# Kernel optimization log

Measured on AMD Instinct MI355X. Metric: run time of the kernel, lower is better.

The kernel has to match this reference:

```python
import jax, jax.numpy as jnp
import numpy as np

B, L, P, A = 32, 512, 128, 128   # batch, prot seq len, prot dim, atom dim
N = 1024                          # total atoms (32 per molecule)
H1, H2 = 512, 256                 # hidden_list


def setup_inputs() -> dict:
    key = jax.random.key(0)
    ks = jax.random.split(key, 12)
    atom_embed = jax.random.normal(ks[0], (N, A), dtype=jnp.float32)
    protSeq_embed = jax.random.normal(ks[1], (B, L, P), dtype=jnp.float32)
    # sorted segment ids, every segment non-empty (32 atoms per molecule)
    atom_splits = jnp.repeat(jnp.arange(B, dtype=jnp.int64), N // B)
    s = 0.05
    att1_W = jax.random.normal(ks[2], (P + A, 128), dtype=jnp.float32) * s
    att1_b = jnp.zeros((128,), dtype=jnp.float32)
    att2_W = jax.random.normal(ks[3], (128, 1), dtype=jnp.float32) * s
    att2_b = jnp.zeros((1,), dtype=jnp.float32)
    d1_W = jax.random.normal(ks[4], (A + P, H1), dtype=jnp.float32) * s
    d1_b = jnp.zeros((H1,), dtype=jnp.float32)
    d2_W = jax.random.normal(ks[5], (H1, H2), dtype=jnp.float32) * s
    d2_b = jnp.zeros((H2,), dtype=jnp.float32)
    out_W = jax.random.normal(ks[6], (H2, 1), dtype=jnp.float32) * s
    out_b = jnp.zeros((1,), dtype=jnp.float32)
    return {"atom_embed": atom_embed, "protSeq_embed": protSeq_embed,
            "atom_splits": atom_splits,
            "att1_W": att1_W, "att1_b": att1_b, "att2_W": att2_W, "att2_b": att2_b,
            "d1_W": d1_W, "d1_b": d1_b, "d2_W": d2_W, "d2_b": d2_b,
            "out_W": out_W, "out_b": out_b}


def reference(atom_embed, protSeq_embed, atom_splits,
              att1_W, att1_b, att2_W, att2_b,
              d1_W, d1_b, d2_W, d2_b, out_W, out_b):
    num_seg = protSeq_embed.shape[0]
    # gather protein rows per atom: [N, L, P]
    prot_g = protSeq_embed[atom_splits]
    # concat with broadcast atom embed: [N, L, P+A]
    atom_x = jnp.broadcast_to(atom_embed[:, None, :], prot_g.shape[:2] + atom_embed.shape[-1:])
    concat = jnp.concatenate([prot_g, atom_x], axis=-1)
    # attention MLP -> scores W: [N, L]
    hid = jnp.tanh(concat @ att1_W + att1_b)
    W = 5.0 * jnp.tanh(hid @ att2_W + att2_b)[..., 0]
    # atom-side weights: exp(max over seq), normalized per segment
    Wc = jnp.exp(jnp.max(W, axis=-1, keepdims=True))                     # [N, 1]
    Sc = jax.ops.segment_sum(Wc, atom_splits, num_segments=num_seg)[atom_splits]
    aa = Wc / Sc                                                          # [N, 1]
    atom_pool = jax.ops.segment_sum(aa * atom_embed, atom_splits, num_segments=num_seg)  # [B, A]
    # protein-side: segment-max scores, softmax over seq, weighted sum
    Wp = jax.ops.segment_max(W, atom_splits, num_segments=num_seg)       # [B, L]
    ap = jax.nn.softmax(Wp, axis=-1)
    prot_pool = jnp.einsum('bl,bld->bd', ap, protSeq_embed)              # [B, P]
    z = jnp.concatenate([atom_pool, prot_pool], axis=-1)
    z = jax.nn.relu(z @ d1_W + d1_b)
    z = jax.nn.relu(z @ d2_W + d2_b)
    return z @ out_W + out_b                                             # [B, 1]
```

## Files before the change

### kernel.cpp

```cpp
#include <hip/hip_runtime.h>
#include <math.h>

#define BSEG 32
#define LSEQ 512

__device__ __forceinline__ float fast_tanh(float x) {
    x = fminf(fmaxf(x, -20.0f), 20.0f);
    float e = __expf(2.0f * x);
    return __fdividef(e - 1.0f, e + 1.0f);
}
__device__ __forceinline__ float trm(float c, float p, float e) {
    return c * __builtin_amdgcn_rcpf(fmaf(p, e, 1.0f));
}
__device__ __forceinline__ float clexp2(float v) {
    return __expf(2.0f * fminf(fmaxf(v, -20.0f), 20.0f));
}

__device__ __forceinline__ void gemm32_exp(
    const float* __restrict__ Xrow0, const float* __restrict__ Wm,
    const float* __restrict__ bias, float* __restrict__ xs,
    float* __restrict__ ws, float* __restrict__ dst, int tid)
{
    #pragma unroll
    for (int t = 0; t < 4; ++t) {
        int flat = (tid + 256 * t) * 4;
        int r = flat >> 7, k4 = flat & 127;
        *(float4*)&xs[r * 132 + k4] = *(const float4*)&Xrow0[r * 128 + k4];
    }
    const int tx = tid & 31, ty = tid >> 5;
    float acc[4][4];
    #pragma unroll
    for (int i = 0; i < 4; ++i)
        #pragma unroll
        for (int j = 0; j < 4; ++j) acc[i][j] = 0.0f;
    #pragma unroll
    for (int q = 0; q < 4; ++q) {
        #pragma unroll
        for (int t = 0; t < 4; ++t) {
            int flat = (tid + 256 * t) * 4;
            int kk = flat >> 7, c4 = flat & 127;
            *(float4*)&ws[kk * 132 + c4] =
                *(const float4*)&Wm[(q * 32 + kk) * 128 + c4];
        }
        __syncthreads();
        #pragma unroll 4
        for (int kk = 0; kk < 32; ++kk) {
            float4 b4 = *(const float4*)&ws[kk * 132 + 4 * tx];
            int k = q * 32 + kk;
            float a0 = xs[(4 * ty + 0) * 132 + k];
            float a1 = xs[(4 * ty + 1) * 132 + k];
            float a2 = xs[(4 * ty + 2) * 132 + k];
            float a3 = xs[(4 * ty + 3) * 132 + k];
            acc[0][0] += a0 * b4.x; acc[0][1] += a0 * b4.y;
            acc[0][2] += a0 * b4.z; acc[0][3] += a0 * b4.w;
            acc[1][0] += a1 * b4.x; acc[1][1] += a1 * b4.y;
            acc[1][2] += a1 * b4.z; acc[1][3] += a1 * b4.w;
            acc[2][0] += a2 * b4.x; acc[2][1] += a2 * b4.y;
            acc[2][2] += a2 * b4.z; acc[2][3] += a2 * b4.w;
            acc[3][0] += a3 * b4.x; acc[3][1] += a3 * b4.y;
            acc[3][2] += a3 * b4.z; acc[3][3] += a3 * b4.w;
        }
        __syncthreads();
    }
    float b4v[4] = {0.f, 0.f, 0.f, 0.f};
    if (bias) *(float4*)b4v = *(const float4*)&bias[4 * tx];
    #pragma unroll
    for (int i = 0; i < 4; ++i) {
        float4 o;
        o.x = clexp2(acc[i][0] + b4v[0]);
        o.y = clexp2(acc[i][1] + b4v[1]);
        o.z = clexp2(acc[i][2] + b4v[2]);
        o.w = clexp2(acc[i][3] + b4v[3]);
        *(float4*)&dst[(4 * ty + i) * 132 + 4 * tx] = o;
    }
}

__global__ __launch_bounds__(256, 2) void fused_kernel(
    const float* __restrict__ atom_embed, const float* __restrict__ protSeq,
    const float* __restrict__ att1_W, const float* __restrict__ att1_b,
    const float* __restrict__ att2_W, const float* __restrict__ att2_b,
    const float* __restrict__ out_b,
    float* __restrict__ pmax, float* __restrict__ zrp,
    float* __restrict__ dpp, float* __restrict__ out)
{
    __shared__ float smem[16896];
    float* eps = smem;
    float* ebs = smem + 4224;
    float* xs  = smem + 8448;
    float* ws  = smem + 12672;
    float* c_s  = smem + 8448;
    float* pmn  = smem + 8576;
    float* wps  = smem + 9664;
    float* es   = smem + 9696;
    float* part = smem + 9728;
    float* scal = smem + 9984;

    const int tid = threadIdx.x;
    const int chunk = blockIdx.x, b = blockIdx.y;
    const int lbase = chunk * 32;

    if (chunk == 0 && tid == 0) out[b] = out_b[0];

    gemm32_exp(protSeq + ((long)(b * 512 + lbase)) * 128, att1_W, att1_b,
               xs, ws, eps, tid);
    gemm32_exp(atom_embed + (long)b * 32 * 128, att1_W + 128 * 128, nullptr,
               xs, ws, ebs, tid);

    if (tid < 128) c_s[tid] = -2.0f * att2_W[tid];
    __syncthreads();
    if (tid < 64) {
        float s = c_s[tid] + c_s[tid + 64];
        #pragma unroll
        for (int m = 1; m < 64; m <<= 1) s += __shfl_xor(s, m);
        if (tid == 0) scal[0] = -0.5f * s + att2_b[0];
    }
    __syncthreads();

    const int ng = tid & 7, lg = tid >> 3;
    const float* qp  = &eps[lg * 132];
    const float* b0p = &ebs[ng * 132];
    const float* b1p = &ebs[(ng + 8) * 132];
    const float* b2p = &ebs[(ng + 16) * 132];
    const float* b3p = &ebs[(ng + 24) * 132];
    float a0 = 0.f, a1 = 0.f, a2 = 0.f, a3 = 0.f;
    #pragma unroll 4
    for (int jj = 0; jj < 128; jj += 4) {
        float4 c4 = *(const float4*)&c_s[jj];
        float4 q  = *(const float4*)(qp + jj);
        float4 b0 = *(const float4*)(b0p + jj);
        float4 b1 = *(const float4*)(b1p + jj);
        float4 b2 = *(const float4*)(b2p + jj);
        float4 b3 = *(const float4*)(b3p + jj);
        a0 += trm(c4.x, q.x, b0.x); a1 += trm(c4.x, q.x, b1.x);
        a2 += trm(c4.x, q.x, b2.x); a3 += trm(c4.x, q.x, b3.x);
        a0 += trm(c4.y, q.y, b0.y); a1 += trm(c4.y, q.y, b1.y);
        a2 += trm(c4.y, q.y, b2.y); a3 += trm(c4.y, q.y, b3.y);
        a0 += trm(c4.z, q.z, b0.z); a1 += trm(c4.z, q.z, b1.z);
        a2 += trm(c4.z, q.z, b2.z); a3 += trm(c4.z, q.z, b3.z);
        a0 += trm(c4.w, q.w, b0.w); a1 += trm(c4.w, q.w, b1.w);
        a2 += trm(c4.w, q.w, b2.w); a3 += trm(c4.w, q.w, b3.w);
    }
    const float bs = scal[0];
    float W0 = 5.0f * fast_tanh(a0 + bs);
    float W1 = 5.0f * fast_tanh(a1 + bs);
    float W2 = 5.0f * fast_tanh(a2 + bs);
    float W3 = 5.0f * fast_tanh(a3 + bs);

    float m = fmaxf(fmaxf(W0, W1), fmaxf(W2, W3));
    #pragma unroll
    for (int d = 1; d < 8; d <<= 1) m = fmaxf(m, __shfl_xor(m, d));
    if (ng == 0) wps[lg] = m;
    pmn[lg * 34 + ng]      = W0;
    pmn[lg * 34 + ng + 8]  = W1;
    pmn[lg * 34 + ng + 16] = W2;
    pmn[lg * 34 + ng + 24] = W3;
    __syncthreads();
    if (tid < 32) {
        float mm = pmn[tid];
        #pragma unroll
        for (int g = 1; g < 32; ++g) mm = fmaxf(mm, pmn[g * 34 + tid]);
        pmax[b * 512 + chunk * 32 + tid] = mm;
        es[tid] = __expf(wps[tid]);
    }
    __syncthreads();
    if (tid < 32) {
        float v = es[tid];
        #pragma unroll
        for (int d = 1; d < 32; d <<= 1) v += __shfl_xor(v, d);
        if (tid == 0) dpp[b * 16 + chunk] = v;
    }
    const int dd = tid & 127, hf = tid >> 7;
    float az = 0.0f;
    #pragma unroll 4
    for (int i = 0; i < 16; ++i)
        az += es[hf * 16 + i] *
              protSeq[((long)(b * 512 + lbase + hf * 16 + i)) * 128 + dd];
    part[tid] = az;
    __syncthreads();
    if (tid < 128) zrp[(b * 16 + chunk) * 128 + tid] = part[tid] + part[128 + tid];
}

__global__ __launch_bounds__(256) void mlp1_kernel(
    const float* __restrict__ pmax, const float* __restrict__ zrp,
    const float* __restrict__ dpp, const float* __restrict__ atom_embed,
    const float* __restrict__ d1_W, const float* __restrict__ d1_b,
    float* __restrict__ h1)
{
    __shared__ float zs[256];
    __shared__ float part[4 * 65];
    __shared__ float expw[32];
    __shared__ float sc[2];
    const int tid = threadIdx.x;
    const int cx = blockIdx.x, b = blockIdx.y;

    if (tid < 32) {
        float m = -1e30f;
        #pragma unroll
        for (int c = 0; c < 16; ++c) m = fmaxf(m, pmax[b * 512 + c * 32 + tid]);
        float e = __expf(m);
        expw[tid] = e;
        #pragma unroll
        for (int d = 1; d < 32; d <<= 1) e += __shfl_xor(e, d);
        if (tid == 0) sc[0] = 1.0f / e;
    }
    if (tid == 64) {
        float s = 0.0f;
        #pragma unroll
        for (int c = 0; c < 16; ++c) s += dpp[b * 16 + c];
        sc[1] = 1.0f / s;
    }
    __syncthreads();
    if (tid < 128) {
        float a = 0.0f;
        #pragma unroll 8
        for (int n = 0; n < 32; ++n)
            a += expw[n] * atom_embed[(b * 32 + n) * 128 + tid];
        zs[tid] = a * sc[0];
    } else {
        int d = tid - 128;
        float a = 0.0f;
        #pragma unroll
        for (int c = 0; c < 16; ++c) a += zrp[(b * 16 + c) * 128 + d];
        zs[tid] = a * sc[1];
    }
    __syncthreads();
    const int c0 = cx * 64, ci = tid & 63, kg = tid >> 6;
    float acc = 0.0f;
    #pragma unroll 8
    for (int k = kg * 64; k < kg * 64 + 64; ++k)
        acc += zs[k] * d1_W[k * 512 + c0 + ci];
    part[kg * 65 + ci] = acc;
    __syncthreads();
    if (tid < 64) {
        float s = part[tid] + part[65 + tid] + part[130 + tid] + part[195 + tid]
                + d1_b[c0 + tid];
        h1[b * 512 + c0 + tid] = fmaxf(s, 0.0f);
    }
}

__global__ __launch_bounds__(256) void mlp2_kernel(
    const float* __restrict__ h1, const float* __restrict__ d2_W,
    const float* __restrict__ d2_b, const float* __restrict__ out_W,
    float* __restrict__ out)
{
    __shared__ float hs[512];
    __shared__ float part[8 * 33];
    const int tid = threadIdx.x;
    const int c0 = blockIdx.x * 32, b = blockIdx.y;
    hs[tid] = h1[b * 512 + tid];
    hs[tid + 256] = h1[b * 512 + 256 + tid];
    __syncthreads();
    const int ci = tid & 31, kg = tid >> 5;
    float acc = 0.0f;
    #pragma unroll 8
    for (int k = kg * 64; k < kg * 64 + 64; ++k)
        acc += hs[k] * d2_W[k * 256 + c0 + ci];
    part[kg * 33 + ci] = acc;
    __syncthreads();
    if (tid < 32) {
        float s = d2_b[c0 + tid];
        #pragma unroll
        for (int g = 0; g < 8; ++g) s += part[g * 33 + tid];
        float contrib = fmaxf(s, 0.0f) * out_W[c0 + tid];
        #pragma unroll
        for (int d = 1; d < 32; d <<= 1) contrib += __shfl_xor(contrib, d);
        if (tid == 0) atomicAdd(&out[b], contrib);
    }
}

extern "C" void kernel_launch(void* const* d_in, const int* in_sizes, int n_in,
                              void* d_out, int out_size, void* d_ws, size_t ws_size,
                              hipStream_t stream) {
    const float* atom_embed = (const float*)d_in[0];
    const float* protSeq    = (const float*)d_in[1];
    const float* att1_W = (const float*)d_in[3];
    const float* att1_b = (const float*)d_in[4];
    const float* att2_W = (const float*)d_in[5];
    const float* att2_b = (const float*)d_in[6];
    const float* d1_W   = (const float*)d_in[7];
    const float* d1_b   = (const float*)d_in[8];
    const float* d2_W   = (const float*)d_in[9];
    const float* d2_b   = (const float*)d_in[10];
    const float* out_W  = (const float*)d_in[11];
    const float* out_b  = (const float*)d_in[12];
    float* out = (float*)d_out;

    float* ws = (float*)d_ws;
    float* pmax = ws;
    float* zrp  = pmax + 16384;
    float* dpp  = zrp + 65536;
    float* h1   = dpp + 512;

    fused_kernel<<<dim3(16, BSEG), 256, 0, stream>>>(
        atom_embed, protSeq, att1_W, att1_b, att2_W, att2_b, out_b,
        pmax, zrp, dpp, out);
    mlp1_kernel<<<dim3(8, BSEG), 256, 0, stream>>>(
        pmax, zrp, dpp, atom_embed, d1_W, d1_b, h1);
    mlp2_kernel<<<dim3(8, BSEG), 256, 0, stream>>>(
        h1, d2_W, d2_b, out_W, out);
}
```

Measured before the change: 123.9 us.

## Hoist atom-side attention GEMM into separate kernel and vectorize LDS A loads

The atom-embedding half of the first attention layer was recomputed by each of the 16 chunk blocks per molecule. It is now computed once per molecule in a new eb_kernel, written to workspace, and loaded by fused_kernel. Separately, the inner GEMM loop now reads A values from shared memory as float4 over groups of four k values, cutting the number of LDS instructions. The cost is an extra kernel launch and a global-memory round trip for the 128x1024 intermediate.

```diff
diff --git a/kernel.cpp b/kernel.cpp
--- a/kernel.cpp
+++ b/kernel.cpp
@@ -19,7 +19,7 @@
 __device__ __forceinline__ void gemm32_exp(
     const float* __restrict__ Xrow0, const float* __restrict__ Wm,
     const float* __restrict__ bias, float* __restrict__ xs,
-    float* __restrict__ ws, float* __restrict__ dst, int tid)
+    float* __restrict__ ws, float* __restrict__ dst, int dstride, int tid)
 {
     #pragma unroll
     for (int t = 0; t < 4; ++t) {
@@ -43,22 +43,22 @@
                 *(const float4*)&Wm[(q * 32 + kk) * 128 + c4];
         }
         __syncthreads();
-        #pragma unroll 4
-        for (int kk = 0; kk < 32; ++kk) {
-            float4 b4 = *(const float4*)&ws[kk * 132 + 4 * tx];
-            int k = q * 32 + kk;
-            float a0 = xs[(4 * ty + 0) * 132 + k];
-            float a1 = xs[(4 * ty + 1) * 132 + k];
-            float a2 = xs[(4 * ty + 2) * 132 + k];
-            float a3 = xs[(4 * ty + 3) * 132 + k];
-            acc[0][0] += a0 * b4.x; acc[0][1] += a0 * b4.y;
-            acc[0][2] += a0 * b4.z; acc[0][3] += a0 * b4.w;
-            acc[1][0] += a1 * b4.x; acc[1][1] += a1 * b4.y;
-            acc[1][2] += a1 * b4.z; acc[1][3] += a1 * b4.w;
-            acc[2][0] += a2 * b4.x; acc[2][1] += a2 * b4.y;
-            acc[2][2] += a2 * b4.z; acc[2][3] += a2 * b4.w;
-            acc[3][0] += a3 * b4.x; acc[3][1] += a3 * b4.y;
-            acc[3][2] += a3 * b4.z; acc[3][3] += a3 * b4.w;
+        #pragma unroll 2
+        for (int kg = 0; kg < 8; ++kg) {
+            float4 A[4];
+            #pragma unroll
+            for (int r = 0; r < 4; ++r)
+                A[r] = *(const float4*)&xs[(4 * ty + r) * 132 + q * 32 + kg * 4];
+            #pragma unroll
+            for (int j = 0; j < 4; ++j) {
+                float4 b4 = *(const float4*)&ws[(kg * 4 + j) * 132 + 4 * tx];
+                #pragma unroll
+                for (int r = 0; r < 4; ++r) {
+                    float av = ((const float*)&A[r])[j];
+                    acc[r][0] += av * b4.x; acc[r][1] += av * b4.y;
+                    acc[r][2] += av * b4.z; acc[r][3] += av * b4.w;
+                }
+            }
         }
         __syncthreads();
     }
@@ -71,12 +71,22 @@
         o.y = clexp2(acc[i][1] + b4v[1]);
         o.z = clexp2(acc[i][2] + b4v[2]);
         o.w = clexp2(acc[i][3] + b4v[3]);
-        *(float4*)&dst[(4 * ty + i) * 132 + 4 * tx] = o;
-    }
+        *(float4*)&dst[(4 * ty + i) * dstride + 4 * tx] = o;
+    }
+}
+
+__global__ __launch_bounds__(256) void eb_kernel(
+    const float* __restrict__ atom_embed, const float* __restrict__ Wa,
+    float* __restrict__ eb)
+{
+    __shared__ float smem[8448];
+    const int b = blockIdx.x;
+    gemm32_exp(atom_embed + (long)b * 32 * 128, Wa, nullptr,
+               smem, smem + 4224, eb + (long)b * 32 * 128, 128, threadIdx.x);
 }
 
 __global__ __launch_bounds__(256, 2) void fused_kernel(
-    const float* __restrict__ atom_embed, const float* __restrict__ protSeq,
+    const float* __restrict__ eb, const float* __restrict__ protSeq,
     const float* __restrict__ att1_W, const float* __restrict__ att1_b,
     const float* __restrict__ att2_W, const float* __restrict__ att2_b,
     const float* __restrict__ out_b,
@@ -101,10 +111,15 @@
 
     if (chunk == 0 && tid == 0) out[b] = out_b[0];
 
+    #pragma unroll
+    for (int t = 0; t < 4; ++t) {
+        int flat = (tid + 256 * t) * 4;
+        int n = flat >> 7, j = flat & 127;
+        *(float4*)&ebs[n * 132 + j] = *(const float4*)&eb[(b * 32 + n) * 128 + j];
+    }
+
     gemm32_exp(protSeq + ((long)(b * 512 + lbase)) * 128, att1_W, att1_b,
-               xs, ws, eps, tid);
-    gemm32_exp(atom_embed + (long)b * 32 * 128, att1_W + 128 * 128, nullptr,
-               xs, ws, ebs, tid);
+               xs, ws, eps, 132, tid);
 
     if (tid < 128) c_s[tid] = -2.0f * att2_W[tid];
     __syncthreads();
@@ -286,13 +301,15 @@
     float* out = (float*)d_out;
 
     float* ws = (float*)d_ws;
-    float* pmax = ws;
+    float* eb   = ws;
+    float* pmax = eb + 131072;
     float* zrp  = pmax + 16384;
     float* dpp  = zrp + 65536;
     float* h1   = dpp + 512;
 
+    eb_kernel<<<BSEG, 256, 0, stream>>>(atom_embed, att1_W + 128 * 128, eb);
     fused_kernel<<<dim3(16, BSEG), 256, 0, stream>>>(
-        atom_embed, protSeq, att1_W, att1_b, att2_W, att2_b, out_b,
+        eb, protSeq, att1_W, att1_b, att2_W, att2_b, out_b,
         pmax, zrp, dpp, out);
     mlp1_kernel<<<dim3(8, BSEG), 256, 0, stream>>>(
         pmax, zrp, dpp, atom_embed, d1_W, d1_b, h1);
```

Measured after the change: 123.9 us. About the same (+0.0%).
